# Kernel optimization log

Hardware: AMD Instinct MI355X
Metric: run time of the kernel (lower is better)

Reference implementation:

```python
import jax, jax.numpy as jnp
import numpy as np

B, H, W, C = 4, 64, 64, 128  # input feature map; num_heads == filters == C


def setup_inputs() -> dict:
    key = jax.random.key(0)
    ks = jax.random.split(key, 5)
    x = jax.random.normal(ks[0], (B, H, W, C), dtype=jnp.float32)
    scale = 0.02  # keep QK^T logits in a sane range for softmax
    Wf = jax.random.normal(ks[1], (C, C), dtype=jnp.float32) * scale
    Wg = jax.random.normal(ks[2], (C, C), dtype=jnp.float32) * scale
    Wh = jax.random.normal(ks[3], (C, C), dtype=jnp.float32) * scale
    Wv = jax.random.normal(ks[4], (C, C), dtype=jnp.float32) * scale
    zeros = jnp.zeros((C,), dtype=jnp.float32)
    return {
        "x": x,
        "Wf": Wf, "bf": zeros,
        "Wg": Wg, "bg": zeros,
        "Wh": Wh, "bh": zeros,
        "Wv": Wv, "bv": zeros,
        "gamma": jnp.float32(0.01),
    }


def reference(x, Wf, bf, Wg, bg, Wh, bh, Wv, bv, gamma):
    b, h, w, c = x.shape
    n = h * w
    xf = x.reshape(b, n, c)  # 1x1 conv == per-pixel linear
    f = xf @ Wf + bf  # [b, n, heads]
    g = xf @ Wg + bg
    v = xf @ Wh + bh
    # full spatial self-attention, unscaled logits (as in the original)
    s = jnp.einsum("bnc,bmc->bnm", f, g)  # [b, n, n]
    att = jax.nn.softmax(s, axis=-1)
    ctx = jnp.einsum("bnm,bmc->bnc", att, v)  # [b, n, heads]
    ctx = gamma * ctx
    # 1x1 conv v (linear activation) + residual
    o = ctx @ Wv + bv + xf
    return o.reshape(b, h, w, -1)
```

## Files before the change

kernel.cpp:

```cpp
#include <hip/hip_runtime.h>
#include <hip/hip_bf16.h>


typedef __hip_bfloat16 bf16;
typedef unsigned char u8;
typedef unsigned int  u32;
typedef unsigned long long u64;
typedef float  floatx4  __attribute__((ext_vector_type(4)));
typedef float  floatx16 __attribute__((ext_vector_type(16)));
typedef short  shortx8 __attribute__((ext_vector_type(8)));
typedef short  shortx4 __attribute__((ext_vector_type(4)));
typedef u32    uintx4  __attribute__((ext_vector_type(4)));
typedef int    intx8   __attribute__((ext_vector_type(8)));

#define CDIM 128
#define NROW 16384
#define NPB  4096
#define LDW  136
#define LDG8 144
#define LDV8 80
#define QTILE 128
#define NKT  64
#define OSCALE 0.125f
#define UNIT_SCALE 0x7F7F7F7F

#define MFMA_QK(a, b, c) \
    __builtin_amdgcn_mfma_scale_f32_16x16x128_f8f6f4((a), (b), (c), 0, 0, \
        0, UNIT_SCALE, 0, UNIT_SCALE)
#define MFMA_PV(a, b, c) \
    __builtin_amdgcn_mfma_scale_f32_32x32x64_f8f6f4((a), (b), (c), 0, 0, \
        0, UNIT_SCALE, 0, UNIT_SCALE)

#define BAR_EXEC() do {                                   \
    asm volatile("" ::: "memory");                        \
    __builtin_amdgcn_s_barrier();                         \
    asm volatile("" ::: "memory");                        \
} while (0)
#define BAR_LDS() do {                                    \
    asm volatile("s_waitcnt lgkmcnt(0)" ::: "memory");    \
    __builtin_amdgcn_s_barrier();                         \
    asm volatile("" ::: "memory");                        \
} while (0)

__device__ __forceinline__ short f2bf(float v) {
    union { __hip_bfloat16 h; short s; } u; u.h = __float2bfloat16(v); return u.s;
}
__device__ __forceinline__ u8 f2fp8(float v) {
    int p = __builtin_amdgcn_cvt_pk_fp8_f32(v, v, 0, false);
    return (u8)(p & 0xff);
}
__device__ __forceinline__ u32 f2fp8x4(float a, float b, float c, float d) {
    int w = __builtin_amdgcn_cvt_pk_fp8_f32(a, b, 0, false);
    w = __builtin_amdgcn_cvt_pk_fp8_f32(c, d, w, true);
    return (u32)w;
}
__device__ __forceinline__ intx8 ld32(const u8* p) {
    uintx4 a = *(const uintx4*)p;
    uintx4 b = *(const uintx4*)(p + 16);
    intx8 r;
    r[0] = (int)a[0]; r[1] = (int)a[1]; r[2] = (int)a[2]; r[3] = (int)a[3];
    r[4] = (int)b[0]; r[5] = (int)b[1]; r[6] = (int)b[2]; r[7] = (int)b[3];
    return r;
}

__global__ __launch_bounds__(256) void proj3_kernel(
    const float* __restrict__ x,
    const float* __restrict__ Wf, const float* __restrict__ bf_,
    const float* __restrict__ Wg, const float* __restrict__ bg_,
    const float* __restrict__ Wh, const float* __restrict__ bh_,
    u8* __restrict__ f8, u8* __restrict__ g8, u8* __restrict__ vT8)
{
    __shared__ bf16 wt[128 * LDW];

    const int t    = threadIdx.x;
    const int wave = t >> 6, lane = t & 63;
    const int quad = lane >> 4, l16 = lane & 15;
    const int mtx    = blockIdx.x >> 8;
    const int rowblk = (blockIdx.x & 255) * 64;
    const int row    = rowblk + wave * 16 + l16;

    const float* Ws[3] = {Wf, Wg, Wh};
    const float* Bs[3] = {bf_, bg_, bh_};
    const float* W    = Ws[mtx];
    const float* bias = Bs[mtx];

    for (int i = t; i < 128 * 32; i += 256) {
        int k = i >> 5, n0 = (i & 31) * 4;
        floatx4 wv = *(const floatx4*)(W + k * CDIM + n0);
#pragma unroll
        for (int j = 0; j < 4; ++j)
            *(short*)&wt[(n0 + j) * LDW + k] = f2bf(wv[j]);
    }

    shortx8 afr[4];
    {
        const float* xp = x + (size_t)row * CDIM + quad * 8;
#pragma unroll
        for (int kc = 0; kc < 4; ++kc) {
            floatx4 u = *(const floatx4*)(xp + kc * 32);
            floatx4 w = *(const floatx4*)(xp + kc * 32 + 4);
            shortx8 a;
            a[0]=f2bf(u[0]); a[1]=f2bf(u[1]); a[2]=f2bf(u[2]); a[3]=f2bf(u[3]);
            a[4]=f2bf(w[0]); a[5]=f2bf(w[1]); a[6]=f2bf(w[2]); a[7]=f2bf(w[3]);
            afr[kc] = a;
        }
    }
    __syncthreads();

    floatx4 acc[8];
#pragma unroll
    for (int nt = 0; nt < 8; ++nt) acc[nt] = (floatx4){0.f, 0.f, 0.f, 0.f};
#pragma unroll
    for (int nt = 0; nt < 8; ++nt) {
        const bf16* wrow = &wt[(nt * 16 + l16) * LDW + quad * 8];
#pragma unroll
        for (int kc = 0; kc < 4; ++kc) {
            shortx8 b = *(const shortx8*)(wrow + kc * 32);
            acc[nt] = __builtin_amdgcn_mfma_f32_16x16x32_bf16(afr[kc], b, acc[nt], 0, 0, 0);
        }
    }

    if (mtx < 2) {
        u8* dst = (mtx == 0) ? f8 : g8;
#pragma unroll
        for (int nt = 0; nt < 8; ++nt) {
            int col = nt * 16 + l16;
            float bv_ = bias[col];
#pragma unroll
            for (int r = 0; r < 4; ++r) {
                int orow = rowblk + wave * 16 + quad * 4 + r;
                dst[(size_t)orow * CDIM + col] = f2fp8(acc[nt][r] + bv_);
            }
        }
    } else {
        __syncthreads();
        u8* vt8 = (u8*)wt;
        const int nloc0 = wave * 16 + quad * 4;
#pragma unroll
        for (int nt = 0; nt < 8; ++nt) {
            int ch = nt * 16 + l16;
            float bv_ = bias[ch];
            *(u32*)&vt8[ch * LDV8 + nloc0] =
                f2fp8x4(acc[nt][0] + bv_, acc[nt][1] + bv_,
                        acc[nt][2] + bv_, acc[nt][3] + bv_);
        }
        __syncthreads();
        const int ch  = t >> 1;
        const int off = (t & 1) * 32;
        const int batch = rowblk >> 12;
        const int n0 = (rowblk & 4095) + off;
        u8* dst = &vT8[((size_t)batch * CDIM + ch) * NPB + n0];
        const u8* src = &vt8[ch * LDV8 + off];
#pragma unroll
        for (int j = 0; j < 2; ++j)
            *(uintx4*)(dst + j * 16) = *(const uintx4*)(src + j * 16);
    }
}

__global__ __launch_bounds__(256, 3) void attn_kernel(
    const u8* __restrict__ f8, const u8* __restrict__ g8,
    const u8* __restrict__ vT8,
    u8* __restrict__ Opart8, float* __restrict__ lbuf, int nsplit)
{
    __shared__ u8 gs8[64 * LDG8];
    __shared__ u8 vs8[128 * LDV8];
    __shared__ u8 ps8[4 * 32 * LDV8];

    const int t    = threadIdx.x;
    const int wave = t >> 6, lane = t & 63;
    const int quad = lane >> 4, l16 = lane & 15;
    const int c31  = lane & 31, hf = lane >> 5;
    const int qg    = blockIdx.x;
    const int split = blockIdx.y;
    const int b  = qg >> 5;
    const int qt = qg & 31;
    const int qbase = b * NPB + qt * QTILE + wave * 32;

    const int kt0 = (split * NKT) / nsplit;
    const int kt1 = ((split + 1) * NKT) / nsplit;

    intx8 qf8[2];
#pragma unroll
    for (int sub = 0; sub < 2; ++sub)
        qf8[sub] = ld32(f8 + (size_t)(qbase + sub * 16 + l16) * CDIM + quad * 32);

    floatx16 o[4];
#pragma unroll
    for (int ct = 0; ct < 4; ++ct)
#pragma unroll
        for (int i = 0; i < 16; ++i) o[ct][i] = 0.f;
    float lacc[2] = {0.f, 0.f};

    const u8* gptr = g8 + (size_t)b * NPB * CDIM;
    const u8* vptr = vT8 + (size_t)b * CDIM * NPB;

    const int gk = t >> 2, go = (t & 3) * 32;
    const int vch = t >> 1, vo = (t & 1) * 32;

    shortx8 gx[2], vx[2];
#pragma unroll
    for (int i = 0; i < 2; ++i) {
        gx[i] = *(const shortx8*)&gptr[(size_t)(kt0 * 64 + gk) * CDIM + go + i * 16];
        vx[i] = *(const shortx8*)&vptr[(size_t)vch * NPB + kt0 * 64 + vo + i * 16];
    }

    for (int kt = kt0; kt < kt1; ++kt) {
        BAR_EXEC();
#pragma unroll
        for (int i = 0; i < 2; ++i) {
            *(shortx8*)&gs8[gk * LDG8 + go + i * 16] = gx[i];
            *(shortx8*)&vs8[vch * LDV8 + vo + i * 16] = vx[i];
        }
        if (kt + 1 < kt1) {
            const int ktn = kt + 1;
#pragma unroll
            for (int i = 0; i < 2; ++i) {
                gx[i] = *(const shortx8*)&gptr[(size_t)(ktn * 64 + gk) * CDIM + go + i * 16];
                vx[i] = *(const shortx8*)&vptr[(size_t)vch * NPB + ktn * 64 + vo + i * 16];
            }
        }
        BAR_LDS();

        floatx4 s[2][4];
#pragma unroll
        for (int nt = 0; nt < 4; ++nt) {
            s[0][nt] = (floatx4){0.f, 0.f, 0.f, 0.f};
            s[1][nt] = (floatx4){0.f, 0.f, 0.f, 0.f};
        }
#pragma unroll
        for (int nt = 0; nt < 4; ++nt) {
            intx8 gf = ld32(&gs8[(nt * 16 + l16) * LDG8 + quad * 32]);
            s[0][nt] = MFMA_QK(gf, qf8[0], s[0][nt]);
            s[1][nt] = MFMA_QK(gf, qf8[1], s[1][nt]);
        }

#pragma unroll
        for (int sub = 0; sub < 2; ++sub) {
            u8* pw = &ps8[(wave * 32 + sub * 16 + l16) * LDV8 + quad * 4];
#pragma unroll
            for (int nt = 0; nt < 4; ++nt) {
                float p0 = __expf(s[sub][nt][0]);
                float p1 = __expf(s[sub][nt][1]);
                float p2 = __expf(s[sub][nt][2]);
                float p3 = __expf(s[sub][nt][3]);
                lacc[sub] += (p0 + p1) + (p2 + p3);
                *(u32*)&pw[nt * 16] = f2fp8x4(p0, p1, p2, p3);
            }
        }

        intx8 pa8 = ld32(&ps8[(wave * 32 + c31) * LDV8 + hf * 32]);

#pragma unroll
        for (int ct = 0; ct < 4; ++ct) {
            intx8 vf = ld32(&vs8[(ct * 32 + c31) * LDV8 + hf * 32]);
            o[ct] = MFMA_PV(pa8, vf, o[ct]);
        }
    }

    const size_t pbase = ((size_t)qg * nsplit + split) * QTILE * CDIM;
#pragma unroll
    for (int ct = 0; ct < 4; ++ct) {
        int col = ct * 32 + c31;
#pragma unroll
        for (int i = 0; i < 16; ++i) {
            int rl = wave * 32 + (i & 3) + 8 * (i >> 2) + 4 * hf;
            Opart8[pbase + (size_t)rl * CDIM + col] = f2fp8(o[ct][i] * OSCALE);
        }
    }
    float* lb = lbuf + ((size_t)qg * nsplit + split) * QTILE;
#pragma unroll
    for (int sub = 0; sub < 2; ++sub) {
        float v = lacc[sub];
        v += __shfl_xor(v, 16);
        v += __shfl_xor(v, 32);
        if (quad == 0) lb[wave * 32 + sub * 16 + l16] = v;
    }
}

__global__ __launch_bounds__(256) void out_kernel(
    const u8* __restrict__ Opart8, const float* __restrict__ lbuf,
    const float* __restrict__ Wv, const float* __restrict__ bv,
    const float* __restrict__ x, const float* __restrict__ gamma,
    float* __restrict__ out, int nsplit)
{
    __shared__ bf16 wt[128 * LDW];

    const int t    = threadIdx.x;
    const int wave = t >> 6, lane = t & 63;
    const int quad = lane >> 4, l16 = lane & 15;
    const int rowblk = blockIdx.x * 64;
    const int row    = rowblk + wave * 16 + l16;

    const float gm = gamma[0];
    for (int i = t; i < 128 * 32; i += 256) {
        int k = i >> 5, n0 = (i & 31) * 4;
        floatx4 wv4 = *(const floatx4*)(Wv + k * CDIM + n0);
#pragma unroll
        for (int j = 0; j < 4; ++j)
            *(short*)&wt[(n0 + j) * LDW + k] = f2bf(wv4[j] * gm);
    }

    const int qg = row >> 7, rl = row & 127;
    float L = 0.f;
    for (int s = 0; s < nsplit; ++s)
        L += lbuf[((size_t)qg * nsplit + s) * QTILE + rl];
    const float inv = 8.0f / L;

    shortx8 afr[4];
#pragma unroll
    for (int kc = 0; kc < 4; ++kc) {
        float a8[8] = {0,0,0,0,0,0,0,0};
        for (int s = 0; s < nsplit; ++s) {
            const u8* p = &Opart8[(((size_t)qg * nsplit + s) * QTILE + rl) * CDIM + quad * 8 + kc * 32];
            u32 lo = *(const u32*)p;
            u32 hi = *(const u32*)(p + 4);
            a8[0] += __builtin_amdgcn_cvt_f32_fp8(lo, 0);
            a8[1] += __builtin_amdgcn_cvt_f32_fp8(lo, 1);
            a8[2] += __builtin_amdgcn_cvt_f32_fp8(lo, 2);
            a8[3] += __builtin_amdgcn_cvt_f32_fp8(lo, 3);
            a8[4] += __builtin_amdgcn_cvt_f32_fp8(hi, 0);
            a8[5] += __builtin_amdgcn_cvt_f32_fp8(hi, 1);
            a8[6] += __builtin_amdgcn_cvt_f32_fp8(hi, 2);
            a8[7] += __builtin_amdgcn_cvt_f32_fp8(hi, 3);
        }
        shortx8 a;
#pragma unroll
        for (int j = 0; j < 8; ++j) a[j] = f2bf(a8[j] * inv);
        afr[kc] = a;
    }
    __syncthreads();

    floatx4 acc[8];
#pragma unroll
    for (int nt = 0; nt < 8; ++nt) acc[nt] = (floatx4){0.f, 0.f, 0.f, 0.f};
#pragma unroll
    for (int nt = 0; nt < 8; ++nt) {
        const bf16* wrow = &wt[(nt * 16 + l16) * LDW + quad * 8];
#pragma unroll
        for (int kc = 0; kc < 4; ++kc) {
            shortx8 b = *(const shortx8*)(wrow + kc * 32);
            acc[nt] = __builtin_amdgcn_mfma_f32_16x16x32_bf16(afr[kc], b, acc[nt], 0, 0, 0);
        }
    }

#pragma unroll
    for (int nt = 0; nt < 8; ++nt) {
        int col = nt * 16 + l16;
        float bias = bv[col];
#pragma unroll
        for (int r = 0; r < 4; ++r) {
            int orow = rowblk + wave * 16 + quad * 4 + r;
            size_t idx = (size_t)orow * CDIM + col;
            out[idx] = acc[nt][r] + bias + x[idx];
        }
    }
}

extern "C" void kernel_launch(void* const* d_in, const int* in_sizes, int n_in,
                              void* d_out, int out_size, void* d_ws, size_t ws_size,
                              hipStream_t stream)
{
    const float* x   = (const float*)d_in[0];
    const float* Wf  = (const float*)d_in[1];
    const float* bf_ = (const float*)d_in[2];
    const float* Wg  = (const float*)d_in[3];
    const float* bg_ = (const float*)d_in[4];
    const float* Wh  = (const float*)d_in[5];
    const float* bh_ = (const float*)d_in[6];
    const float* Wv  = (const float*)d_in[7];
    const float* bv  = (const float*)d_in[8];
    const float* gm  = (const float*)d_in[9];
    float* out = (float*)d_out;

    const size_t need6 = (size_t)3 * NROW * CDIM
                       + (size_t)128 * 6 * QTILE * CDIM
                       + (size_t)128 * 6 * QTILE * 4;
    const int nsplit = (ws_size >= need6) ? 6 : 4;

    u8*   f8    = (u8*)d_ws;
    u8*   g8    = f8 + (size_t)NROW * CDIM;
    u8*   vT8   = g8 + (size_t)NROW * CDIM;
    u8*   Opart8 = vT8 + (size_t)NROW * CDIM;
    float* lbuf = (float*)(Opart8 + (size_t)128 * nsplit * QTILE * CDIM);

    proj3_kernel<<<768, 256, 0, stream>>>(x, Wf, bf_, Wg, bg_, Wh, bh_, f8, g8, vT8);
    attn_kernel<<<dim3(128, nsplit), 256, 0, stream>>>(f8, g8, vT8, Opart8, lbuf, nsplit);
    out_kernel<<<256, 256, 0, stream>>>(Opart8, lbuf, Wv, bv, x, gm, out, nsplit);
}
```

Before: 132.7 us.

## Use 32x32 MFMA for QK and pass P to PV in registers via lane shuffles

```diff
diff --git a/kernel.cpp b/kernel.cpp
--- a/kernel.cpp
+++ b/kernel.cpp
@@ -9,7 +9,6 @@
 typedef float  floatx4  __attribute__((ext_vector_type(4)));
 typedef float  floatx16 __attribute__((ext_vector_type(16)));
 typedef short  shortx8 __attribute__((ext_vector_type(8)));
-typedef short  shortx4 __attribute__((ext_vector_type(4)));
 typedef u32    uintx4  __attribute__((ext_vector_type(4)));
 typedef int    intx8   __attribute__((ext_vector_type(8)));
 
@@ -24,10 +23,7 @@
 #define OSCALE 0.125f
 #define UNIT_SCALE 0x7F7F7F7F
 
-#define MFMA_QK(a, b, c) \
-    __builtin_amdgcn_mfma_scale_f32_16x16x128_f8f6f4((a), (b), (c), 0, 0, \
-        0, UNIT_SCALE, 0, UNIT_SCALE)
-#define MFMA_PV(a, b, c) \
+#define MFMA32(a, b, c) \
     __builtin_amdgcn_mfma_scale_f32_32x32x64_f8f6f4((a), (b), (c), 0, 0, \
         0, UNIT_SCALE, 0, UNIT_SCALE)
 
@@ -164,11 +160,9 @@
 {
     __shared__ u8 gs8[64 * LDG8];
     __shared__ u8 vs8[128 * LDV8];
-    __shared__ u8 ps8[4 * 32 * LDV8];
 
     const int t    = threadIdx.x;
     const int wave = t >> 6, lane = t & 63;
-    const int quad = lane >> 4, l16 = lane & 15;
     const int c31  = lane & 31, hf = lane >> 5;
     const int qg    = blockIdx.x;
     const int split = blockIdx.y;
@@ -179,17 +173,17 @@
     const int kt0 = (split * NKT) / nsplit;
     const int kt1 = ((split + 1) * NKT) / nsplit;
 
-    intx8 qf8[2];
-#pragma unroll
-    for (int sub = 0; sub < 2; ++sub)
-        qf8[sub] = ld32(f8 + (size_t)(qbase + sub * 16 + l16) * CDIM + quad * 32);
+    intx8 qb[2];
+#pragma unroll
+    for (int half = 0; half < 2; ++half)
+        qb[half] = ld32(f8 + (size_t)(qbase + c31) * CDIM + half * 64 + hf * 32);
 
     floatx16 o[4];
 #pragma unroll
     for (int ct = 0; ct < 4; ++ct)
 #pragma unroll
         for (int i = 0; i < 16; ++i) o[ct][i] = 0.f;
-    float lacc[2] = {0.f, 0.f};
+    float lacc = 0.f;
 
     const u8* gptr = g8 + (size_t)b * NPB * CDIM;
     const u8* vptr = vT8 + (size_t)b * CDIM * NPB;
@@ -221,39 +215,43 @@
         }
         BAR_LDS();
 
-        floatx4 s[2][4];
-#pragma unroll
-        for (int nt = 0; nt < 4; ++nt) {
-            s[0][nt] = (floatx4){0.f, 0.f, 0.f, 0.f};
-            s[1][nt] = (floatx4){0.f, 0.f, 0.f, 0.f};
-        }
-#pragma unroll
-        for (int nt = 0; nt < 4; ++nt) {
-            intx8 gf = ld32(&gs8[(nt * 16 + l16) * LDG8 + quad * 32]);
-            s[0][nt] = MFMA_QK(gf, qf8[0], s[0][nt]);
-            s[1][nt] = MFMA_QK(gf, qf8[1], s[1][nt]);
-        }
-
-#pragma unroll
-        for (int sub = 0; sub < 2; ++sub) {
-            u8* pw = &ps8[(wave * 32 + sub * 16 + l16) * LDV8 + quad * 4];
-#pragma unroll
-            for (int nt = 0; nt < 4; ++nt) {
-                float p0 = __expf(s[sub][nt][0]);
-                float p1 = __expf(s[sub][nt][1]);
-                float p2 = __expf(s[sub][nt][2]);
-                float p3 = __expf(s[sub][nt][3]);
-                lacc[sub] += (p0 + p1) + (p2 + p3);
-                *(u32*)&pw[nt * 16] = f2fp8x4(p0, p1, p2, p3);
+        floatx16 s32[2];
+#pragma unroll
+        for (int h = 0; h < 2; ++h) {
+#pragma unroll
+            for (int i = 0; i < 16; ++i) s32[h][i] = 0.f;
+            intx8 ga0 = ld32(&gs8[(h * 32 + c31) * LDG8 + hf * 32]);
+            s32[h] = MFMA32(ga0, qb[0], s32[h]);
+            intx8 ga1 = ld32(&gs8[(h * 32 + c31) * LDG8 + 64 + hf * 32]);
+            s32[h] = MFMA32(ga1, qb[1], s32[h]);
+        }
+
+        u32 pk[2][4];
+#pragma unroll
+        for (int h = 0; h < 2; ++h)
+#pragma unroll
+            for (int g = 0; g < 4; ++g) {
+                float e0 = __expf(s32[h][4 * g + 0]);
+                float e1 = __expf(s32[h][4 * g + 1]);
+                float e2 = __expf(s32[h][4 * g + 2]);
+                float e3 = __expf(s32[h][4 * g + 3]);
+                lacc += (e0 + e1) + (e2 + e3);
+                pk[h][g] = f2fp8x4(e0, e1, e2, e3);
             }
-        }
-
-        intx8 pa8 = ld32(&ps8[(wave * 32 + c31) * LDV8 + hf * 32]);
+
+        intx8 pa;
+#pragma unroll
+        for (int g = 0; g < 4; ++g) {
+            u32 sw0 = (u32)__shfl_xor((int)pk[0][g], 32);
+            u32 sw1 = (u32)__shfl_xor((int)pk[1][g], 32);
+            pa[2 * g]     = hf ? (int)sw1      : (int)pk[0][g];
+            pa[2 * g + 1] = hf ? (int)pk[1][g] : (int)sw0;
+        }
 
 #pragma unroll
         for (int ct = 0; ct < 4; ++ct) {
             intx8 vf = ld32(&vs8[(ct * 32 + c31) * LDV8 + hf * 32]);
-            o[ct] = MFMA_PV(pa8, vf, o[ct]);
+            o[ct] = MFMA32(pa, vf, o[ct]);
         }
     }
 
@@ -268,12 +266,9 @@
         }
     }
     float* lb = lbuf + ((size_t)qg * nsplit + split) * QTILE;
-#pragma unroll
-    for (int sub = 0; sub < 2; ++sub) {
-        float v = lacc[sub];
-        v += __shfl_xor(v, 16);
-        v += __shfl_xor(v, 32);
-        if (quad == 0) lb[wave * 32 + sub * 16 + l16] = v;
+    {
+        float v = lacc + __shfl_xor(lacc, 32);
+        if (hf == 0) lb[wave * 32 + c31] = v;
     }
 }
 
```

After: 133.2 us. Within noise of the previous version (+0.4%).
